# Kernel optimization log

Measured on AMD Instinct MI355X. Metric: run time of the kernel, lower is better.

The kernel has to match this reference:

```python
import jax, jax.numpy as jnp
import numpy as np

ORDER = 5
NB_DF = 96
LOOKAHEAD = 0


def setup_inputs() -> dict:
    key = jax.random.key(0)
    k1, k2 = jax.random.split(key)
    B, T, F = 32, 2000, 481
    spec = jax.random.normal(k1, (B, 1, T, F, 2), dtype=jnp.float32)
    coefs = jax.random.normal(k2, (B, ORDER, T, NB_DF, 2), dtype=jnp.float32)
    return {"spec": spec, "coefs": coefs}


def reference(spec, coefs):
    # spec: [B,1,T,F,2], coefs: [B,order,T,nb_df,2]
    B, C, T, F, _ = spec.shape
    # real/imag of the deep-filtered frequency band only ([B,1,T,nb_df])
    sr = spec[..., :NB_DF, 0]
    si = spec[..., :NB_DF, 1]
    pad_before = ORDER - 1 - LOOKAHEAD
    pad_cfg = ((0, 0), (0, 0), (pad_before, LOOKAHEAD), (0, 0))
    sr_p = jnp.pad(sr, pad_cfg)
    si_p = jnp.pad(si, pad_cfg)
    # unfold over time: lag n window = padded[:, :, n:n+T]  -> [order,B,1,T,nb_df]
    sur = jnp.stack([sr_p[:, :, n:n + T] for n in range(ORDER)], axis=0)
    sui = jnp.stack([si_p[:, :, n:n + T] for n in range(ORDER)], axis=0)
    # coefs viewed as [B,1,order,T,nb_df] -> align as [order,B,1,T,nb_df]
    cr = jnp.transpose(coefs[..., 0], (1, 0, 2, 3))[:, :, None]
    ci = jnp.transpose(coefs[..., 1], (1, 0, 2, 3))[:, :, None]
    # complex contraction over the order (time-lag) axis
    out_r = jnp.sum(sur * cr - sui * ci, axis=0)  # [B,1,T,nb_df]
    out_i = jnp.sum(sur * ci + sui * cr, axis=0)
    spec_f = jnp.stack([out_r, out_i], axis=-1)   # [B,1,T,nb_df,2]
    # write filtered band back into the full spectrogram
    return spec.at[..., :NB_DF, :].set(spec_f)
```

## Files before the change

kernel.cpp:

```cpp
#include <hip/hip_runtime.h>


constexpr int ORDER = 5;
constexpr int NB_DF = 96;
constexpr int T_DIM = 2000;
constexpr int F_DIM = 481;
constexpr int B_DIM = 32;

constexpr int TCHUNK = 25;
constexpr int NCHUNK = T_DIM / TCHUNK;
constexpr int F4     = NB_DF / 2;
constexpr int BLOCK  = 256;

constexpr int FIR_THREADS = B_DIM * NCHUNK * F4;
constexpr int FIR_BLOCKS  = FIR_THREADS / BLOCK;

constexpr int COPY_BLOCKS = 3616;
constexpr int COPY_F      = F_DIM - NB_DF;
constexpr int N_ROWS      = B_DIM * T_DIM;
constexpr unsigned COPY_ELEMS = (unsigned)N_ROWS * (unsigned)COPY_F;

__global__ __launch_bounds__(BLOCK) void ApplyDF_29231547416739_kernel(
    const float2* __restrict__ spec,
    const float4* __restrict__ coefs4,
    float2* __restrict__ out)
{
    const int bid = blockIdx.x;
    const int tid = threadIdx.x;

    if (bid < FIR_BLOCKS) {
        const int flat  = bid * BLOCK + tid;
        const int col   = flat % F4;
        const int chunk = flat / F4;
        const int b     = chunk / NCHUNK;
        const int t0    = (chunk % NCHUNK) * TCHUNK;

        const size_t bT = (size_t)b * T_DIM;

        const float2* sp = spec + (bT + t0) * F_DIM + col * 2;
        float2*       op = out  + (bT + t0) * F_DIM + col * 2;

        const float4* cp[ORDER];
#pragma unroll
        for (int n = 0; n < ORDER; ++n)
            cp[n] = coefs4 + ((bT * ORDER) + (size_t)n * T_DIM + t0) * F4 + col;

        float4 w[ORDER];
#pragma unroll
        for (int j = 0; j < ORDER - 1; ++j) {
            float4 v = make_float4(0.f, 0.f, 0.f, 0.f);
            const int tt = t0 - (ORDER - 1) + j;
            if (tt >= 0) {
                const float2* p = sp + (j - (ORDER - 1)) * F_DIM;
                const float2 lo = p[0], hi = p[1];
                v = make_float4(lo.x, lo.y, hi.x, hi.y);
            }
            w[j] = v;
        }

        for (int g = 0; g < TCHUNK / ORDER; ++g) {
#pragma unroll
            for (int r = 0; r < ORDER; ++r) {
                {
                    const float2 lo = sp[0], hi = sp[1];
                    w[(r + ORDER - 1) % ORDER] = make_float4(lo.x, lo.y, hi.x, hi.y);
                }
                float4 acc = make_float4(0.f, 0.f, 0.f, 0.f);
#pragma unroll
                for (int n = 0; n < ORDER; ++n) {
                    const float4 c = *cp[n];
                    const float4 s4 = w[(r + n) % ORDER];
                    acc.x = fmaf(s4.x, c.x, fmaf(-s4.y, c.y, acc.x));
                    acc.y = fmaf(s4.x, c.y, fmaf( s4.y, c.x, acc.y));
                    acc.z = fmaf(s4.z, c.z, fmaf(-s4.w, c.w, acc.z));
                    acc.w = fmaf(s4.z, c.w, fmaf( s4.w, c.z, acc.w));
                }
                op[0] = make_float2(acc.x, acc.y);
                op[1] = make_float2(acc.z, acc.w);
                sp += F_DIM;
                op += F_DIM;
#pragma unroll
                for (int n = 0; n < ORDER; ++n) cp[n] += F4;
            }
        }
    } else {
        unsigned i = (unsigned)(bid - FIR_BLOCKS) * BLOCK + tid;
        const unsigned stride = (unsigned)COPY_BLOCKS * BLOCK;
        for (; i < COPY_ELEMS; i += stride) {
            const unsigned row = i / COPY_F;
            const unsigned ff  = i - row * COPY_F + NB_DF;
            const size_t off = (size_t)row * F_DIM + ff;
            out[off] = spec[off];
        }
    }
}

extern "C" void kernel_launch(void* const* d_in, const int* in_sizes, int n_in,
                              void* d_out, int out_size, void* d_ws, size_t ws_size,
                              hipStream_t stream) {
    const float2* spec   = (const float2*)d_in[0];
    const float4* coefs4 = (const float4*)d_in[1];
    float2* out = (float2*)d_out;

    dim3 grid(FIR_BLOCKS + COPY_BLOCKS);
    dim3 block(BLOCK);
    ApplyDF_29231547416739_kernel<<<grid, block, 0, stream>>>(spec, coefs4, out);
}
```

Measured before the change: 573.1 us.

## Give each FIR output its own thread and interleave unrolled copy blocks

The FIR part now assigns one thread to each (batch, time, column-pair) output. Each thread loads its five lagged spectrum rows and five coefficient vectors directly, replacing the per-thread sequential walk over a 25-frame time chunk. FIR and copy blocks alternate by block-index parity. The copy path is unrolled into fixed batches of four independent loads, with a tail for the leftover elements. The aim is far more threads and memory-level parallelism for a bandwidth-bound kernel. The cost is that each spectrum row is re-read by several threads, which relies on cache hits.

Measured after the change: 551.7 us. 1.04x faster.

```diff
diff --git a/kernel.cpp b/kernel.cpp
--- a/kernel.cpp
+++ b/kernel.cpp
@@ -7,89 +7,85 @@
 constexpr int F_DIM = 481;
 constexpr int B_DIM = 32;
 
-constexpr int TCHUNK = 25;
-constexpr int NCHUNK = T_DIM / TCHUNK;
-constexpr int F4     = NB_DF / 2;
-constexpr int BLOCK  = 256;
+constexpr int F4    = NB_DF / 2;
+constexpr int BLOCK = 256;
 
-constexpr int FIR_THREADS = B_DIM * NCHUNK * F4;
+constexpr int FIR_THREADS = B_DIM * T_DIM * F4;
 constexpr int FIR_BLOCKS  = FIR_THREADS / BLOCK;
 
-constexpr int COPY_BLOCKS = 3616;
+constexpr int COPY_BLOCKS = FIR_BLOCKS;
 constexpr int COPY_F      = F_DIM - NB_DF;
 constexpr int N_ROWS      = B_DIM * T_DIM;
-constexpr unsigned COPY_ELEMS = (unsigned)N_ROWS * (unsigned)COPY_F;
+constexpr unsigned COPY_ELEMS  = (unsigned)N_ROWS * (unsigned)COPY_F;
+constexpr unsigned COPY_STRIDE = (unsigned)COPY_BLOCKS * BLOCK;
 
-__global__ __launch_bounds__(BLOCK) void ApplyDF_29231547416739_kernel(
+__global__ __launch_bounds__(BLOCK, 6) void ApplyDF_29231547416739_kernel(
     const float2* __restrict__ spec,
     const float4* __restrict__ coefs4,
     float2* __restrict__ out)
 {
     const int bid = blockIdx.x;
     const int tid = threadIdx.x;
+    const int half = bid >> 1;
 
-    if (bid < FIR_BLOCKS) {
-        const int flat  = bid * BLOCK + tid;
-        const int col   = flat % F4;
-        const int chunk = flat / F4;
-        const int b     = chunk / NCHUNK;
-        const int t0    = (chunk % NCHUNK) * TCHUNK;
+    if ((bid & 1) == 0) {
+        const int flat = half * BLOCK + tid;
+        const int col  = flat % F4;
+        const int rest = flat / F4;
+        const int b    = rest / T_DIM;
+        const int t    = rest - b * T_DIM;
 
-        const size_t bT = (size_t)b * T_DIM;
-
-        const float2* sp = spec + (bT + t0) * F_DIM + col * 2;
-        float2*       op = out  + (bT + t0) * F_DIM + col * 2;
-
-        const float4* cp[ORDER];
+        float2 slo[ORDER], shi[ORDER];
+#pragma unroll
+        for (int n = 0; n < ORDER; ++n) {
+            const int tt  = t + n - (ORDER - 1);
+            const int ttc = tt >= 0 ? tt : 0;
+            const float2* p = spec + ((size_t)b * T_DIM + ttc) * F_DIM + 2 * col;
+            float2 lo = p[0];
+            float2 hi = p[1];
+            if (tt < 0) { lo = make_float2(0.f, 0.f); hi = make_float2(0.f, 0.f); }
+            slo[n] = lo; shi[n] = hi;
+        }
+        float4 c[ORDER];
 #pragma unroll
         for (int n = 0; n < ORDER; ++n)
-            cp[n] = coefs4 + ((bT * ORDER) + (size_t)n * T_DIM + t0) * F4 + col;
+            c[n] = coefs4[(((size_t)b * ORDER + n) * T_DIM + t) * F4 + col];
 
-        float4 w[ORDER];
+        float4 acc = make_float4(0.f, 0.f, 0.f, 0.f);
 #pragma unroll
-        for (int j = 0; j < ORDER - 1; ++j) {
-            float4 v = make_float4(0.f, 0.f, 0.f, 0.f);
-            const int tt = t0 - (ORDER - 1) + j;
-            if (tt >= 0) {
-                const float2* p = sp + (j - (ORDER - 1)) * F_DIM;
-                const float2 lo = p[0], hi = p[1];
-                v = make_float4(lo.x, lo.y, hi.x, hi.y);
-            }
-            w[j] = v;
+        for (int n = 0; n < ORDER; ++n) {
+            acc.x = fmaf(slo[n].x, c[n].x, fmaf(-slo[n].y, c[n].y, acc.x));
+            acc.y = fmaf(slo[n].x, c[n].y, fmaf( slo[n].y, c[n].x, acc.y));
+            acc.z = fmaf(shi[n].x, c[n].z, fmaf(-shi[n].y, c[n].w, acc.z));
+            acc.w = fmaf(shi[n].x, c[n].w, fmaf( shi[n].y, c[n].z, acc.w));
         }
 
-        for (int g = 0; g < TCHUNK / ORDER; ++g) {
+        float2* op = out + ((size_t)b * T_DIM + t) * F_DIM + 2 * col;
+        op[0] = make_float2(acc.x, acc.y);
+        op[1] = make_float2(acc.z, acc.w);
+    } else {
+        const unsigned base = (unsigned)half * BLOCK + tid;
 #pragma unroll
-            for (int r = 0; r < ORDER; ++r) {
-                {
-                    const float2 lo = sp[0], hi = sp[1];
-                    w[(r + ORDER - 1) % ORDER] = make_float4(lo.x, lo.y, hi.x, hi.y);
-                }
-                float4 acc = make_float4(0.f, 0.f, 0.f, 0.f);
+        for (int rep = 0; rep < 2; ++rep) {
+            const unsigned i0 = base + (unsigned)(rep * 4) * COPY_STRIDE;
+            size_t off[4];
+            float2 v[4];
 #pragma unroll
-                for (int n = 0; n < ORDER; ++n) {
-                    const float4 c = *cp[n];
-                    const float4 s4 = w[(r + n) % ORDER];
-                    acc.x = fmaf(s4.x, c.x, fmaf(-s4.y, c.y, acc.x));
-                    acc.y = fmaf(s4.x, c.y, fmaf( s4.y, c.x, acc.y));
-                    acc.z = fmaf(s4.z, c.z, fmaf(-s4.w, c.w, acc.z));
-                    acc.w = fmaf(s4.z, c.w, fmaf( s4.w, c.z, acc.w));
-                }
-                op[0] = make_float2(acc.x, acc.y);
-                op[1] = make_float2(acc.z, acc.w);
-                sp += F_DIM;
-                op += F_DIM;
+            for (int u = 0; u < 4; ++u) {
+                const unsigned idx = i0 + (unsigned)u * COPY_STRIDE;
+                const unsigned row = idx / COPY_F;
+                const unsigned ff  = idx - row * COPY_F + NB_DF;
+                off[u] = (size_t)row * F_DIM + ff;
+                v[u]   = spec[off[u]];
+            }
 #pragma unroll
-                for (int n = 0; n < ORDER; ++n) cp[n] += F4;
-            }
+            for (int u = 0; u < 4; ++u) out[off[u]] = v[u];
         }
-    } else {
-        unsigned i = (unsigned)(bid - FIR_BLOCKS) * BLOCK + tid;
-        const unsigned stride = (unsigned)COPY_BLOCKS * BLOCK;
-        for (; i < COPY_ELEMS; i += stride) {
-            const unsigned row = i / COPY_F;
-            const unsigned ff  = i - row * COPY_F + NB_DF;
-            const size_t off = (size_t)row * F_DIM + ff;
+        if (base < 64000u) {
+            const unsigned idx = base + 8u * COPY_STRIDE;
+            const unsigned row = idx / COPY_F;
+            const unsigned ff  = idx - row * COPY_F + NB_DF;
+            const size_t off   = (size_t)row * F_DIM + ff;
             out[off] = spec[off];
         }
     }
```
